# Kernel tuning notes

Measured on AMD Instinct MI355X. Metric: run time of the kernel, lower is better.

## Reference

```python
import jax, jax.numpy as jnp
import numpy as np

N, E, G = 20000, 320000, 256
FXD, FXT, OD = 78, 954, 128


def _lin(key, fan_in, fan_out, scale=0.05):
    return jax.random.normal(key, (fan_in, fan_out), dtype=jnp.float32) * scale


def setup_inputs() -> dict:
    key = jax.random.key(0)
    ks = jax.random.split(key, 24)
    inp = {
        "x1": jax.random.normal(ks[0], (N, FXD), dtype=jnp.float32),
        "edge_index1": jax.random.randint(ks[1], (2, E), 0, N, dtype=jnp.int32),
        "batch1": (jnp.arange(N, dtype=jnp.int32) * G) // N,  # sorted, every graph non-empty
        "x2": jax.random.normal(ks[2], (N, FXD), dtype=jnp.float32),
        "edge_index2": jax.random.randint(ks[3], (2, E), 0, N, dtype=jnp.int32),
        "batch2": (jnp.arange(N, dtype=jnp.int32) * G) // N,
        "cell": jax.random.normal(ks[4], (G, FXT), dtype=jnp.float32),
        # GCNConv weights (shared across the two drug branches, as in the module)
        "Wc1": _lin(ks[5], FXD, FXD), "bc1": jnp.zeros((FXD,), jnp.float32),
        "Wc2": _lin(ks[6], FXD, FXD * 2), "bc2": jnp.zeros((FXD * 2,), jnp.float32),
        "Wc3": _lin(ks[7], FXD * 2, FXD * 4), "bc3": jnp.zeros((FXD * 4,), jnp.float32),
        "Wg1": _lin(ks[8], FXD * 4, FXD * 2), "bg1": jnp.zeros((FXD * 2,), jnp.float32),
        "Wg2": _lin(ks[9], FXD * 2, OD), "bg2": jnp.zeros((OD,), jnp.float32),
        # cell reduction MLP 954 -> 2048 -> 512 -> 256
        "Wr1": _lin(ks[10], FXT, 2048), "br1": jnp.zeros((2048,), jnp.float32),
        "Wr2": _lin(ks[11], 2048, 512), "br2": jnp.zeros((512,), jnp.float32),
        "Wr3": _lin(ks[12], 512, OD * 2), "br3": jnp.zeros((OD * 2,), jnp.float32),
        # head MLP 512 -> 1024 -> 512 -> 128 -> 2
        "Wf1": _lin(ks[13], OD * 4, 1024), "bf1": jnp.zeros((1024,), jnp.float32),
        "Wf2": _lin(ks[14], 1024, 512), "bf2": jnp.zeros((512,), jnp.float32),
        "Wf3": _lin(ks[15], 512, 128), "bf3": jnp.zeros((128,), jnp.float32),
        "Wo": _lin(ks[16], 128, 2), "bo": jnp.zeros((2,), jnp.float32),
    }
    return inp


def gcn_conv(x, W, b, src, dst, n):
    """PyG GCNConv: h = D^{-1/2}(A+I)D^{-1/2} (x W) + b (self-loops added)."""
    h = x @ W
    loops = jnp.arange(n, dtype=src.dtype)
    s = jnp.concatenate([src, loops])
    d = jnp.concatenate([dst, loops])
    deg = jax.ops.segment_sum(jnp.ones_like(s, dtype=h.dtype), d, num_segments=n)
    dinv = jax.lax.rsqrt(deg)  # deg >= 1 due to self-loops
    norm = dinv[s] * dinv[d]  # [E+N]
    out = jax.ops.segment_sum(h[s] * norm[:, None], d, num_segments=n)
    return out + b


def drug_branch(x, ei, batch, Wc1, bc1, Wc2, bc2, Wc3, bc3, Wg1, bg1, Wg2, bg2):
    src, dst = ei[0], ei[1]
    n = x.shape[0]
    x = jax.nn.relu(gcn_conv(x, Wc1, bc1, src, dst, n))
    x = jax.nn.relu(gcn_conv(x, Wc2, bc2, src, dst, n))
    x = jax.nn.relu(gcn_conv(x, Wc3, bc3, src, dst, n))
    x = jax.ops.segment_max(x, batch, num_segments=G)  # global max pool -> [G, 312]
    x = jax.nn.relu(x @ Wg1 + bg1)
    x = x @ Wg2 + bg2  # dropout is identity in eval mode
    return x


def reference(x1, edge_index1, batch1, x2, edge_index2, batch2, cell,
              Wc1, bc1, Wc2, bc2, Wc3, bc3, Wg1, bg1, Wg2, bg2,
              Wr1, br1, Wr2, br2, Wr3, br3,
              Wf1, bf1, Wf2, bf2, Wf3, bf3, Wo, bo):
    g1 = drug_branch(x1, edge_index1, batch1, Wc1, bc1, Wc2, bc2, Wc3, bc3, Wg1, bg1, Wg2, bg2)
    g2 = drug_branch(x2, edge_index2, batch2, Wc1, bc1, Wc2, bc2, Wc3, bc3, Wg1, bg1, Wg2, bg2)
    # F.normalize(cell, p=2, dim=1)
    cv = cell / jnp.maximum(jnp.linalg.norm(cell, axis=1, keepdims=True), 1e-12)
    cv = jax.nn.relu(cv @ Wr1 + br1)
    cv = jax.nn.relu(cv @ Wr2 + br2)
    cv = jax.nn.relu(cv @ Wr3 + br3)
    xc = jnp.concatenate([g1, g2, cv], axis=1)  # [G, 512]
    xc = jax.nn.relu(xc @ Wf1 + bf1)
    xc = jax.nn.relu(xc @ Wf2 + bf2)
    xc = jax.nn.relu(xc @ Wf3 + bf3)
    return xc @ Wo + bo  # [G, 2]
```

## Files before the change

kernel.cpp:

```cpp
#include <hip/hip_runtime.h>

#define N_NODES 20000
#define N_EDGES 320000
#define N_GRAPH 256
#define ECHUNK 2048
#define DCAP 64

__device__ __forceinline__ ushort f2b(float f) {
  unsigned u = __float_as_uint(f);
  u += 0x7FFFu + ((u >> 16) & 1u);
  return (ushort)(u >> 16);
}
__device__ __forceinline__ float b2f(ushort u) {
  return __uint_as_float(((unsigned)u) << 16);
}

typedef __attribute__((ext_vector_type(8))) short bf16x8;
typedef __attribute__((ext_vector_type(4))) float f32x4;

__device__ __forceinline__ void acc8(float* a, uint4 u) {
  a[0] += __uint_as_float(u.x << 16);
  a[1] += __uint_as_float(u.x & 0xFFFF0000u);
  a[2] += __uint_as_float(u.y << 16);
  a[3] += __uint_as_float(u.y & 0xFFFF0000u);
  a[4] += __uint_as_float(u.z << 16);
  a[5] += __uint_as_float(u.z & 0xFFFF0000u);
  a[6] += __uint_as_float(u.w << 16);
  a[7] += __uint_as_float(u.w & 0xFFFF0000u);
}

template <int BN_T>
__launch_bounds__(256)
__global__ void gemm_fused(const ushort* __restrict__ h,
                           const int* __restrict__ cnt,
                           const ushort* __restrict__ col_idx,
                           const float* __restrict__ dinv,
                           const ushort* __restrict__ Bt, int ldbt,
                           ushort* __restrict__ C, int ldc,
                           const float* __restrict__ bias,
                           int Nr, int M, int cwz) {
  constexpr int BM = 64, BN = BN_T * 16, LA = 104;
  __shared__ __align__(16) ushort Afull[BM][LA];
  __shared__ __align__(16) ushort Bsl[BN][40];
  const int tid = threadIdx.x;
  const int R = (Nr + BM - 1) / BM;
  const int RR = (R + 7) >> 3;
  const int xz = blockIdx.x & 7, g = blockIdx.x >> 3;
  const int by = xz * RR + g;
  if (by >= R) return;
  const int row0 = by * BM;
  const int lane = tid & 63, w = tid >> 6;
  const uint4* hv = (const uint4*)h;

  for (int task = tid; task < BM * 10; task += 256) {
    const int r = task / 10, c = task - r * 10;
    const int n = row0 + r;
    uint4 val = make_uint4(0u, 0u, 0u, 0u);
    if (n < Nr) {
      float a[8] = {};
      acc8(a, hv[(size_t)n * 10 + c]);
      const int beg = n << 6;
      const int end = beg + min(cnt[n], DCAP);
      int e = beg;
      for (; e + 3 < end; e += 4) {
        int s0 = col_idx[e], s1 = col_idx[e + 1];
        int s2 = col_idx[e + 2], s3 = col_idx[e + 3];
        acc8(a, hv[(size_t)s0 * 10 + c]); acc8(a, hv[(size_t)s1 * 10 + c]);
        acc8(a, hv[(size_t)s2 * 10 + c]); acc8(a, hv[(size_t)s3 * 10 + c]);
      }
      for (; e < end; ++e) acc8(a, hv[(size_t)col_idx[e] * 10 + c]);
      const float dn = dinv[n];
      ushort o[8];
#pragma unroll
      for (int j = 0; j < 8; ++j) o[j] = f2b(dn * a[j]);
      val = *(uint4*)o;
    }
    *(uint4*)&Afull[r][c * 8] = val;
  }
  for (int task = tid; task < BM * 2; task += 256) {
    const int r = task >> 1, c2 = task & 1;
    *(uint4*)&Afull[r][80 + c2 * 8] = make_uint4(0u, 0u, 0u, 0u);
  }
  __syncthreads();

  f32x4 acc[BN_T] = {};
  const int mrow = w * 16;
  const int lm = lane & 15, lq = (lane >> 4) * 8;
  for (int t = 0; t < 3; ++t) {
    const int k0 = t * 32;
    for (int s = tid; s < BN * 4; s += 256) {
      const int br = s >> 2, bo = (s & 3) * 8;
      *(uint4*)&Bsl[br][bo] = *(const uint4*)&Bt[(size_t)br * ldbt + k0 + bo];
    }
    __syncthreads();
    bf16x8 af = *(const bf16x8*)&Afull[mrow + lm][k0 + lq];
#pragma unroll
    for (int nt = 0; nt < BN_T; ++nt) {
      bf16x8 bf = *(const bf16x8*)&Bsl[nt * 16 + lm][lq];
      acc[nt] = __builtin_amdgcn_mfma_f32_16x16x32_bf16(af, bf, acc[nt], 0, 0, 0);
    }
    __syncthreads();
  }

  const int rquad = (lane >> 4) * 4;
#pragma unroll
  for (int nt = 0; nt < BN_T; ++nt) {
    const int cc = nt * 16 + lm;
    if (cc >= cwz) continue;
    const bool cval = cc < M;
    const float bv = cval ? bias[cc] : 0.f;
#pragma unroll
    for (int r = 0; r < 4; ++r) {
      const int rr = row0 + mrow + rquad + r;
      if (rr >= Nr) continue;
      float v = cval ? fmaxf(acc[nt][r] + bv, 0.f) * dinv[rr] : 0.f;
      C[(size_t)rr * ldc + cc] = f2b(v);
    }
  }
}

template <int POOL>
__launch_bounds__(256)
__global__ void gemm_mfma(const ushort* __restrict__ A, int lda,
                          const ushort* __restrict__ Bt, int ldbt,
                          void* __restrict__ Cv, int ldc,
                          const float* __restrict__ bias,
                          int Nr, int Kpad, int M, int do_relu, int obf,
                          const float* __restrict__ dsc, int cwz,
                          const int* __restrict__ bA, const int* __restrict__ bB,
                          int nsplit, int gA, int gB, int gTot) {
  constexpr int BM = 128, BN = 128, BK = 32, LK = 40;
  __shared__ __align__(16) ushort Asl[BM][LK];
  __shared__ __align__(16) ushort Bsl[BN][LK];
  const int tid = threadIdx.x;
  const int Cc = (M + BN - 1) / BN;
  const int R = (Nr + BM - 1) / BM;
  const int RR = (R + 7) >> 3;
  const int xz = blockIdx.x & 7, g = blockIdx.x >> 3;
  const int q = g / Cc;
  const int by = xz * RR + q, bx = g - q * Cc;
  if (by >= R) return;
  const int row0 = by * BM, col0 = bx * BN;

  const int lane = tid & 63, w = tid >> 6;
  const int a_r = tid >> 1, a_h = tid & 1;

  const int nst = Kpad / BK;

  uint4 pa0, pa1, pb0, pb1;
  auto load_tile = [&](int k0) {
    if (row0 + a_r < Nr) {
      const uint4* p = (const uint4*)(A + (size_t)(row0 + a_r) * lda + k0 + a_h * 16);
      pa0 = p[0]; pa1 = p[1];
    } else {
      pa0 = make_uint4(0u, 0u, 0u, 0u); pa1 = pa0;
    }
    const uint4* pq = (const uint4*)(Bt + (size_t)(col0 + a_r) * ldbt + k0 + a_h * 16);
    pb0 = pq[0]; pb1 = pq[1];
  };
  auto commit = [&]() {
    *(uint4*)&Asl[a_r][a_h * 16] = pa0;
    *(uint4*)&Asl[a_r][a_h * 16 + 8] = pa1;
    *(uint4*)&Bsl[a_r][a_h * 16] = pb0;
    *(uint4*)&Bsl[a_r][a_h * 16 + 8] = pb1;
  };

  f32x4 acc[2][8] = {};
  const int mrow = w * 32;
  const int lm = lane & 15, lq = (lane >> 4) * 8;

  load_tile(0);
  for (int t = 0; t < nst; ++t) {
    commit();
    __syncthreads();
    if (t + 1 < nst) load_tile((t + 1) * BK);
    bf16x8 af0 = *(const bf16x8*)&Asl[mrow + lm][lq];
    bf16x8 af1 = *(const bf16x8*)&Asl[mrow + 16 + lm][lq];
#pragma unroll
    for (int nt = 0; nt < 8; ++nt) {
      bf16x8 bf = *(const bf16x8*)&Bsl[nt * 16 + lm][lq];
      acc[0][nt] = __builtin_amdgcn_mfma_f32_16x16x32_bf16(af0, bf, acc[0][nt], 0, 0, 0);
      acc[1][nt] = __builtin_amdgcn_mfma_f32_16x16x32_bf16(af1, bf, acc[1][nt], 0, 0, 0);
    }
    __syncthreads();
  }

  const int rquad = (lane >> 4) * 4;

  if constexpr (POOL) {
    __shared__ int Ps[4][BN];
    for (int idx = tid; idx < 4 * BN; idx += 256) Ps[idx >> 7][idx & 127] = 0;
    __syncthreads();
    const int g0 = (row0 < nsplit) ? gA + bA[row0] : gB + bB[row0 - nsplit];
    int gr8[2][4];
#pragma unroll
    for (int mt = 0; mt < 2; ++mt)
#pragma unroll
      for (int r = 0; r < 4; ++r) {
        const int rr = row0 + mrow + mt * 16 + rquad + r;
        gr8[mt][r] = (rr < Nr)
                         ? ((rr < nsplit) ? gA + bA[rr] : gB + bB[rr - nsplit])
                         : -1;
      }
#pragma unroll
    for (int mt = 0; mt < 2; ++mt)
#pragma unroll
      for (int nt = 0; nt < 8; ++nt) {
        const int cl = nt * 16 + lm;
        if (col0 + cl >= M) continue;
        const float bv = bias[col0 + cl];
#pragma unroll
        for (int r = 0; r < 4; ++r) {
          const int gg = gr8[mt][r];
          if (gg < 0) continue;
          const float v = fmaxf(acc[mt][nt][r] + bv, 0.f);
          atomicMax(&Ps[gg - g0][cl], __float_as_int(v));
        }
      }
    __syncthreads();
    for (int idx = tid; idx < 4 * BN; idx += 256) {
      const int s = idx >> 7, c = idx & 127;
      const int gg = g0 + s, cc = col0 + c;
      if (gg < gTot && cc < M)
        atomicMax((int*)Cv + (size_t)gg * ldc + cc, Ps[s][c]);
    }
    return;
  }

  const int cz = (cwz > M) ? cwz : M;
#pragma unroll
  for (int mt = 0; mt < 2; ++mt) {
#pragma unroll
    for (int nt = 0; nt < 8; ++nt) {
      const int cc = col0 + nt * 16 + lm;
      if (cc >= cz) continue;
      const bool cval = cc < M;
      const float bv = (cval && bias) ? bias[cc] : 0.f;
#pragma unroll
      for (int r = 0; r < 4; ++r) {
        const int rr = row0 + mrow + mt * 16 + rquad + r;
        if (rr >= Nr) continue;
        float v = cval ? (acc[mt][nt][r] + bv) : 0.f;
        if (do_relu) v = fmaxf(v, 0.f);
        if (dsc) v *= dsc[rr];
        if (obf) ((ushort*)Cv)[(size_t)rr * ldc + cc] = f2b(v);
        else     ((float*)Cv)[(size_t)rr * ldc + cc] = v;
      }
    }
  }
}

struct GJob {
  const void* A; const ushort* Bt; void* C; const float* bias;
  int lda, a_f32, ldbt, ldc, Nr, Kpad, M, relu, obf, rsplit, cpad, rb, cb, blk0;
};

__launch_bounds__(256)
__global__ void gemm_grp(GJob j0, GJob j1, int njobs) {
  GJob j = (njobs > 1 && (int)blockIdx.x >= j1.blk0) ? j1 : j0;
  const int local = blockIdx.x - j.blk0;
  const int by = local / j.cb, bx = local - by * j.cb;
  const int row0 = by * 32, col0 = bx * 64;
  const int tid = threadIdx.x, lane = tid & 63, w = tid >> 6;

  __shared__ __align__(16) char smem[32768];
  ushort (*Asl)[32][40] = (ushort (*)[32][40])smem;
  ushort (*Bsl)[64][40] = (ushort (*)[64][40])(smem + 10240);
  float  (*Rs)[32][64]  = (float  (*)[32][64])smem;

  const int a_r = lane >> 1, a_h = lane & 1;
  const int lm = lane & 15, lq = (lane >> 4) * 8;
  const int nst = j.Kpad / 32;

  uint4 ra[4], rb[4];
  auto gload = [&](int t) {
    const int k0 = t * 32;
    const int ar = row0 + a_r;
    if (j.a_f32) {
      if (ar < j.Nr) {
        const uint4* p = (const uint4*)((const float*)j.A + (size_t)ar * j.lda + k0 + a_h * 16);
        ra[0] = p[0]; ra[1] = p[1]; ra[2] = p[2]; ra[3] = p[3];
      } else {
        ra[0] = make_uint4(0u, 0u, 0u, 0u); ra[1] = ra[0]; ra[2] = ra[0]; ra[3] = ra[0];
      }
    } else {
      if (ar < j.Nr) {
        const uint4* p = (const uint4*)((const ushort*)j.A + (size_t)ar * j.lda + k0 + a_h * 16);
        ra[0] = p[0]; ra[1] = p[1];
      } else {
        ra[0] = make_uint4(0u, 0u, 0u, 0u); ra[1] = ra[0];
      }
    }
    const uint4* q = (const uint4*)(j.Bt + (size_t)(col0 + lane) * j.ldbt + k0);
    rb[0] = q[0]; rb[1] = q[1]; rb[2] = q[2]; rb[3] = q[3];
  };
  auto commit = [&]() {
    if (j.a_f32) {
      ushort tmp[16];
      const float* f = (const float*)&ra[0];
#pragma unroll
      for (int q2 = 0; q2 < 16; ++q2) tmp[q2] = f2b(f[q2]);
      *(uint4*)&Asl[w][a_r][a_h * 16]     = *(uint4*)&tmp[0];
      *(uint4*)&Asl[w][a_r][a_h * 16 + 8] = *(uint4*)&tmp[8];
    } else {
      *(uint4*)&Asl[w][a_r][a_h * 16]     = ra[0];
      *(uint4*)&Asl[w][a_r][a_h * 16 + 8] = ra[1];
    }
    *(uint4*)&Bsl[w][lane][0]  = rb[0];
    *(uint4*)&Bsl[w][lane][8]  = rb[1];
    *(uint4*)&Bsl[w][lane][16] = rb[2];
    *(uint4*)&Bsl[w][lane][24] = rb[3];
  };

  f32x4 acc[2][4] = {};
  if (w < nst) {
    gload(w);
    for (int t = w; t < nst; t += 4) {
      commit();
      bf16x8 af0 = *(const bf16x8*)&Asl[w][lm][lq];
      bf16x8 af1 = *(const bf16x8*)&Asl[w][16 + lm][lq];
      bf16x8 bq0 = *(const bf16x8*)&Bsl[w][lm][lq];
      bf16x8 bq1 = *(const bf16x8*)&Bsl[w][16 + lm][lq];
      bf16x8 bq2 = *(const bf16x8*)&Bsl[w][32 + lm][lq];
      bf16x8 bq3 = *(const bf16x8*)&Bsl[w][48 + lm][lq];
      if (t + 4 < nst) gload(t + 4);
      acc[0][0] = __builtin_amdgcn_mfma_f32_16x16x32_bf16(af0, bq0, acc[0][0], 0, 0, 0);
      acc[0][1] = __builtin_amdgcn_mfma_f32_16x16x32_bf16(af0, bq1, acc[0][1], 0, 0, 0);
      acc[0][2] = __builtin_amdgcn_mfma_f32_16x16x32_bf16(af0, bq2, acc[0][2], 0, 0, 0);
      acc[0][3] = __builtin_amdgcn_mfma_f32_16x16x32_bf16(af0, bq3, acc[0][3], 0, 0, 0);
      acc[1][0] = __builtin_amdgcn_mfma_f32_16x16x32_bf16(af1, bq0, acc[1][0], 0, 0, 0);
      acc[1][1] = __builtin_amdgcn_mfma_f32_16x16x32_bf16(af1, bq1, acc[1][1], 0, 0, 0);
      acc[1][2] = __builtin_amdgcn_mfma_f32_16x16x32_bf16(af1, bq2, acc[1][2], 0, 0, 0);
      acc[1][3] = __builtin_amdgcn_mfma_f32_16x16x32_bf16(af1, bq3, acc[1][3], 0, 0, 0);
    }
  }

  __syncthreads();
  const int rquad = (lane >> 4) * 4;
#pragma unroll
  for (int mt = 0; mt < 2; ++mt)
#pragma unroll
    for (int nt = 0; nt < 4; ++nt)
#pragma unroll
      for (int r = 0; r < 4; ++r)
        Rs[w][mt * 16 + rquad + r][nt * 16 + lm] = acc[mt][nt][r];
  __syncthreads();

  const int rrow = tid >> 3, cs = (tid & 7) * 8;
  float v[8];
  {
    float4 x0 = *(const float4*)&Rs[0][rrow][cs];
    float4 x1 = *(const float4*)&Rs[0][rrow][cs + 4];
    v[0] = x0.x; v[1] = x0.y; v[2] = x0.z; v[3] = x0.w;
    v[4] = x1.x; v[5] = x1.y; v[6] = x1.z; v[7] = x1.w;
  }
#pragma unroll
  for (int ww = 1; ww < 4; ++ww) {
    float4 x0 = *(const float4*)&Rs[ww][rrow][cs];
    float4 x1 = *(const float4*)&Rs[ww][rrow][cs + 4];
    v[0] += x0.x; v[1] += x0.y; v[2] += x0.z; v[3] += x0.w;
    v[4] += x1.x; v[5] += x1.y; v[6] += x1.z; v[7] += x1.w;
  }
  const int rg = row0 + rrow;
  if (rg < j.Nr) {
    int rm = rg, rq = 0;
    if (j.rsplit) { rq = rg / j.rsplit; rm = rg - rq * j.rsplit; }
#pragma unroll
    for (int q = 0; q < 8; ++q) {
      const int cc = col0 + cs + q;
      if (cc >= j.cpad) break;
      float x = 0.f;
      if (cc < j.M) {
        x = v[q] + j.bias[cc];
        if (j.relu) x = fmaxf(x, 0.f);
      }
      const size_t di = (size_t)rm * j.ldc + (size_t)rq * j.M + cc;
      if (j.obf) ((ushort*)j.C)[di] = f2b(x);
      else       ((float*)j.C)[di] = x;
    }
  }
}

struct WJob { const float* W; ushort* T; int Mv, Kv, Mp, Kp, blk0; };
struct WArgs {
  WJob j[11]; int wblocks; const float* cell; ushort* cv;
  const int* e1; const int* e2; int* cnt; ushort* col; int E, npass, rng, scatB;
};

__launch_bounds__(256)
__global__ void prep_all(WArgs a) {
  const int bid = blockIdx.x, tid = threadIdx.x;
  if (bid < a.wblocks) {
    __shared__ float t[32][33];
    int ji = 0;
#pragma unroll
    for (int i = 1; i < 11; ++i)
      if (bid >= a.j[i].blk0) ji = i;
    WJob wj = a.j[ji];
    const int lt = bid - wj.blk0;
    const int ktiles = wj.Kp >> 5;
    const int tn = lt / ktiles, tk = lt - tn * ktiles;
    const int n0 = tn << 5, k0 = tk << 5;
    const int c = tid & 31, r = tid >> 5;
    const int nn = n0 + c;
#pragma unroll
    for (int i = 0; i < 4; ++i) {
      const int k = k0 + r + i * 8;
      t[r + i * 8][c] = (k < wj.Kv && nn < wj.Mv) ? wj.W[(size_t)k * wj.Mv + nn] : 0.f;
    }
    __syncthreads();
    const int k = k0 + c;
#pragma unroll
    for (int i = 0; i < 4; ++i) {
      const int n = n0 + r + i * 8;
      wj.T[(size_t)n * wj.Kp + k] = f2b(t[c][r + i * 8]);
    }
    return;
  }
  if (bid < a.wblocks + N_GRAPH) {
    __shared__ float red[256];
    const int g = bid - a.wblocks;
    const float* row = a.cell + (size_t)g * 954;
    float s = 0.f;
    for (int f = tid; f < 954; f += 256) { float vv = row[f]; s += vv * vv; }
    red[tid] = s;
    __syncthreads();
    for (int off2 = 128; off2 > 0; off2 >>= 1) {
      if (tid < off2) red[tid] += red[tid + off2];
      __syncthreads();
    }
    const float inv = 1.f / fmaxf(sqrtf(red[0]), 1e-12f);
    ushort* orow = a.cv + (size_t)g * 960;
    for (int f = tid; f < 954; f += 256) orow[f] = f2b(row[f] * inv);
    for (int f = 954 + tid; f < 960; f += 256) orow[f] = 0;
    return;
  }
  const int sb = bid - a.wblocks - N_GRAPH;
  const int xcd = sb & 7;
  const int lo = xcd * a.rng, hi = lo + a.rng;
  const int base = (sb >> 3) * ECHUNK;
  const int TE = a.npass * a.E;
  for (int i = tid; i < ECHUNK; i += 256) {
    int e = base + i;
    if (e >= TE) break;
    int d, s;
    if (e < a.E) { d = a.e1[a.E + e]; s = a.e1[e]; }
    else { int jj = e - a.E; d = N_NODES + a.e2[a.E + jj]; s = N_NODES + a.e2[jj]; }
    if (d >= lo && d < hi) {
      int p = atomicAdd(&a.cnt[d], 1);
      if (p < DCAP) a.col[((size_t)d << 6) + p] = (ushort)s;
    }
  }
}

__global__ void scatterb_kernel(const int* __restrict__ e1, const int* __restrict__ e2,
                                int* __restrict__ cnt, ushort* __restrict__ col_idx,
                                int E, int npass, int rng) {
  const int xcd = blockIdx.x & 7;
  const int lo = xcd * rng, hi = lo + rng;
  const int base = (blockIdx.x >> 3) * ECHUNK;
  const int TE = npass * E;
  for (int i = threadIdx.x; i < ECHUNK; i += 256) {
    int e = base + i;
    if (e >= TE) break;
    int d, s;
    if (e < E) { d = e1[E + e]; s = e1[e]; }
    else { int jj = e - E; d = N_NODES + e2[E + jj]; s = N_NODES + e2[jj]; }
    if (d >= lo && d < hi) {
      int p = atomicAdd(&cnt[d], 1);
      if (p < DCAP) col_idx[((size_t)d << 6) + p] = (ushort)s;
    }
  }
}

__global__ void dinv_cvt_kernel(const int* __restrict__ cnt, float* __restrict__ dinv,
                                const float* __restrict__ xa, const float* __restrict__ xb,
                                int nsplit, ushort* __restrict__ dst, int total) {
  int gid = blockIdx.x * blockDim.x + threadIdx.x;
  if (gid >= total) return;
  int n = gid / 10, v = gid - n * 10;
  const float sc = rsqrtf((float)(cnt[n] + 1));
  if (v == 0) dinv[n] = sc;
  const float* src = (n < nsplit) ? xa + (size_t)n * 78 : xb + (size_t)(n - nsplit) * 78;
  const int f0 = v * 8;
  ushort o[8];
#pragma unroll
  for (int jj = 0; jj < 8; ++jj)
    o[jj] = (f0 + jj < 78) ? f2b(src[f0 + jj] * sc) : 0;
  ((uint4*)(dst + (size_t)n * 80))[v] = *(uint4*)o;
}

__global__ void aggb_flat(const ushort* __restrict__ h, const int* __restrict__ cnt,
                          const ushort* __restrict__ col_idx, const float* __restrict__ dinv,
                          ushort* __restrict__ out, int in_ld, int out_ld,
                          int V, int total) {
  int gid = blockIdx.x * blockDim.x + threadIdx.x;
  if (gid >= total) return;
  int n = gid / V, v = gid - n * V;
  const uint4* hv = (const uint4*)h;
  const int ivs = in_ld >> 3;
  float a[8] = {};
  acc8(a, hv[(size_t)n * ivs + v]);
  const int beg = n << 6;
  const int end = beg + min(cnt[n], DCAP);
  int e = beg;
  for (; e + 3 < end; e += 4) {
    int s0 = col_idx[e], s1 = col_idx[e + 1], s2 = col_idx[e + 2], s3 = col_idx[e + 3];
    uint4 u0 = hv[(size_t)s0 * ivs + v], u1 = hv[(size_t)s1 * ivs + v];
    uint4 u2 = hv[(size_t)s2 * ivs + v], u3 = hv[(size_t)s3 * ivs + v];
    acc8(a, u0); acc8(a, u1); acc8(a, u2); acc8(a, u3);
  }
  for (; e < end; ++e)
    acc8(a, hv[(size_t)col_idx[e] * ivs + v]);
  const float din = dinv[n];
  ushort o[8];
#pragma unroll
  for (int jj = 0; jj < 8; ++jj) o[jj] = f2b(din * a[jj]);
  ((uint4*)(out + (size_t)n * out_ld))[v] = *(uint4*)o;
}

__global__ void wo_kernel(const float* __restrict__ wf3o, const float* __restrict__ Wo,
                          const float* __restrict__ bo, float* __restrict__ out) {
  int gid = blockIdx.x * blockDim.x + threadIdx.x;
  if (gid >= N_GRAPH * 2) return;
  int row = gid >> 1, col = gid & 1;
  float v = bo[col];
  const float* a = wf3o + (size_t)row * 128;
  for (int k = 0; k < 128; ++k) v += a[k] * Wo[k * 2 + col];
  out[gid] = v;
}

extern "C" void kernel_launch(void* const* d_in, const int* in_sizes, int n_in,
                              void* d_out, int out_size, void* d_ws, size_t ws_size,
                              hipStream_t stream) {
  (void)in_sizes; (void)n_in; (void)out_size;
  const float* x1  = (const float*)d_in[0];
  const int*   ei1 = (const int*)d_in[1];
  const int*   bt1 = (const int*)d_in[2];
  const float* x2  = (const float*)d_in[3];
  const int*   ei2 = (const int*)d_in[4];
  const int*   bt2 = (const int*)d_in[5];
  const float* cell = (const float*)d_in[6];
  const float* Wc1 = (const float*)d_in[7];  const float* bc1 = (const float*)d_in[8];
  const float* Wc2 = (const float*)d_in[9];  const float* bc2 = (const float*)d_in[10];
  const float* Wc3 = (const float*)d_in[11]; const float* bc3 = (const float*)d_in[12];
  const float* Wg1 = (const float*)d_in[13]; const float* bg1 = (const float*)d_in[14];
  const float* Wg2 = (const float*)d_in[15]; const float* bg2 = (const float*)d_in[16];
  const float* Wr1 = (const float*)d_in[17]; const float* br1 = (const float*)d_in[18];
  const float* Wr2 = (const float*)d_in[19]; const float* br2 = (const float*)d_in[20];
  const float* Wr3 = (const float*)d_in[21]; const float* br3 = (const float*)d_in[22];
  const float* Wf1 = (const float*)d_in[23]; const float* bf1 = (const float*)d_in[24];
  const float* Wf2 = (const float*)d_in[25]; const float* bf2 = (const float*)d_in[26];
  const float* Wf3 = (const float*)d_in[27]; const float* bf3 = (const float*)d_in[28];
  const float* Wo  = (const float*)d_in[29]; const float* bo  = (const float*)d_in[30];
  float* out = (float*)d_out;

  const bool batched = ws_size >= (size_t)95 * 1024 * 1024;
  const int NPASS = batched ? 2 : 1;
  const int NN = NPASS * N_NODES;

  char* ws = (char*)d_ws;
  size_t off = 0;
  auto alloc_f = [&](size_t ne) {
    ne = (ne + 3) & ~(size_t)3;
    float* p = (float*)(ws + off); off += ne * 4; return p;
  };
  auto alloc_i = [&](size_t ne) {
    ne = (ne + 3) & ~(size_t)3;
    int* p = (int*)(ws + off); off += ne * 4; return p;
  };
  ushort* xb16w = (ushort*)alloc_f((size_t)NN * 80);
  ushort* ab16  = (ushort*)alloc_f((size_t)NN * 80);
  ushort* xb16s = (ushort*)alloc_f((size_t)NN * 40);
  float* dinv   = alloc_f(NN);
  int* cnt      = alloc_i(NN);
  float* pooled = alloc_f((size_t)512 * 320);
  ushort* cv16  = (ushort*)alloc_f((size_t)N_GRAPH * 480);
  ushort* wg1o  = (ushort*)alloc_f((size_t)512 * 80);
  ushort* wr1o  = (ushort*)alloc_f((size_t)256 * 1024);
  ushort* wr2o  = (ushort*)alloc_f((size_t)256 * 256);
  ushort* catbuf = (ushort*)alloc_f((size_t)256 * 256);
  ushort* wf1o  = (ushort*)alloc_f((size_t)256 * 512);
  ushort* wf2o  = (ushort*)alloc_f((size_t)256 * 256);
  float* wf3o   = alloc_f((size_t)256 * 128);
  ushort* wc1t  = (ushort*)alloc_f(128 * 96 / 2);
  ushort* wc2t  = (ushort*)alloc_f(192 * 96 / 2);
  ushort* wc3t  = (ushort*)alloc_f(384 * 160 / 2);
  ushort* wr1t  = (ushort*)alloc_f(2048 * 960 / 2);
  ushort* wr2t  = (ushort*)alloc_f(512 * 2048 / 2);
  ushort* wf1t  = (ushort*)alloc_f(1024 * 512 / 2);
  ushort* wg1t  = (ushort*)alloc_f(192 * 320 / 2);
  ushort* wg2t  = (ushort*)alloc_f(128 * 160 / 2);
  ushort* wr3t  = (ushort*)alloc_f(256 * 512 / 2);
  ushort* wf2t  = (ushort*)alloc_f(512 * 1024 / 2);
  ushort* wf3t  = (ushort*)alloc_f(128 * 512 / 2);
  ushort* col_idx = (ushort*)alloc_i((size_t)NN * DCAP / 2);

  auto mfma_pool = [&](const ushort* A, int lda, const ushort* Bt, int ldbt,
                       const float* bias, int Nr, int Kpad, int M,
                       const int* bA, const int* bB, int nsplit, int gA, int gB, int gTot) {
    int Cc = (M + 127) / 128, R = (Nr + 127) / 128, RR = (R + 7) >> 3;
    dim3 grid(8 * RR * Cc, 1, 1);
    gemm_mfma<1><<<grid, 256, 0, stream>>>(A, lda, Bt, ldbt, pooled, 320, bias,
                                           Nr, Kpad, M, 1, 0, nullptr, 0,
                                           bA, bB, nsplit, gA, gB, gTot);
  };
  auto mkjob = [&](const void* A, int lda, int a_f32, const ushort* Bt, int ldbt,
                   void* C, int ldc, const float* bias, int Nr, int Kpad, int M,
                   int relu, int obf, int rsplit, int cpad) {
    GJob g; g.A = A; g.Bt = Bt; g.C = C; g.bias = bias;
    g.lda = lda; g.a_f32 = a_f32; g.ldbt = ldbt; g.ldc = ldc;
    g.Nr = Nr; g.Kpad = Kpad; g.M = M; g.relu = relu; g.obf = obf;
    g.rsplit = rsplit; g.cpad = cpad;
    g.rb = (Nr + 31) / 32; g.cb = (M + 63) / 64; g.blk0 = 0;
    return g;
  };
  auto grp1 = [&](GJob a) {
    gemm_grp<<<a.rb * a.cb, 256, 0, stream>>>(a, a, 1);
  };
  auto grp2 = [&](GJob a, GJob b) {
    b.blk0 = a.rb * a.cb;
    gemm_grp<<<b.blk0 + b.rb * b.cb, 256, 0, stream>>>(a, b, 2);
  };

  WArgs wa{};
  int wb = 0;
  {
    int nj = 0;
    auto addw = [&](const float* W, ushort* T, int Mv, int Kv, int Mp, int Kp) {
      wa.j[nj].W = W; wa.j[nj].T = T; wa.j[nj].Mv = Mv; wa.j[nj].Kv = Kv;
      wa.j[nj].Mp = Mp; wa.j[nj].Kp = Kp; wa.j[nj].blk0 = wb;
      wb += (Mp >> 5) * (Kp >> 5); ++nj;
    };
    addw(Wc1, wc1t,   78,   78,  128,   96);
    addw(Wc2, wc2t,  156,   78,  192,   96);
    addw(Wc3, wc3t,  312,  156,  384,  160);
    addw(Wr1, wr1t, 2048,  954, 2048,  960);
    addw(Wr2, wr2t,  512, 2048,  512, 2048);
    addw(Wf1, wf1t, 1024,  512, 1024,  512);
    addw(Wg1, wg1t,  156,  312,  192,  320);
    addw(Wg2, wg2t,  128,  156,  128,  160);
    addw(Wr3, wr3t,  256,  512,  256,  512);
    addw(Wf2, wf2t,  512, 1024,  512, 1024);
    addw(Wf3, wf3t,  128,  512,  128,  512);
    wa.wblocks = wb; wa.cell = cell; wa.cv = cv16;
  }

  auto node_layers = [&](const float* xa, const float* xb,
                         const int* bta, const int* btb, int npass, int pool_base) {
    const int nn = npass * N_NODES;
    {
      int tot = nn * 10;
      dinv_cvt_kernel<<<(tot + 255) / 256, 256, 0, stream>>>(
          cnt, dinv, xa, xb, (npass == 2) ? N_NODES : nn, xb16s, tot);
    }
    const int R = (nn + 63) / 64, RR = (R + 7) >> 3;
    dim3 fgrid(8 * RR, 1, 1);
    gemm_fused<8><<<fgrid, 256, 0, stream>>>(xb16s, cnt, col_idx, dinv, wc1t, 96,
                                             (ushort*)ab16, 80, bc1, nn, 78, 80);
    gemm_fused<12><<<fgrid, 256, 0, stream>>>((ushort*)ab16, cnt, col_idx, dinv, wc2t, 96,
                                              xb16w, 160, bc2, nn, 156, 160);
    {
      int tot = nn * 20;
      aggb_flat<<<(tot + 255) / 256, 256, 0, stream>>>(xb16w, cnt, col_idx, dinv,
                                                       (ushort*)ab16, 160, 160, 20, tot);
    }
    mfma_pool((ushort*)ab16, 160, wc3t, 160, bc3, nn, 160, 312,
              bta, btb, (npass == 2) ? N_NODES : nn,
              pool_base, pool_base + N_GRAPH, pool_base + npass * N_GRAPH);
  };

  if (batched) {
    const int echunks = (2 * N_EDGES + ECHUNK - 1) / ECHUNK;
    hipMemsetAsync(cnt, 0, (size_t)NN * 4 + (size_t)512 * 320 * 4, stream);
    wa.e1 = ei1; wa.e2 = ei2; wa.cnt = cnt; wa.col = col_idx;
    wa.E = N_EDGES; wa.npass = 2; wa.rng = NN / 8; wa.scatB = 8 * echunks;
    prep_all<<<wb + N_GRAPH + wa.scatB, 256, 0, stream>>>(wa);
    node_layers(x1, x2, bt1, bt2, 2, 0);
  } else {
    wa.e1 = ei1; wa.e2 = ei1; wa.cnt = cnt; wa.col = col_idx;
    wa.E = N_EDGES; wa.npass = 1; wa.rng = N_NODES / 8; wa.scatB = 0;
    prep_all<<<wb + N_GRAPH, 256, 0, stream>>>(wa);
    const int echunks = (N_EDGES + ECHUNK - 1) / ECHUNK;
    hipMemsetAsync(cnt, 0, (size_t)N_NODES * 4 + (size_t)512 * 320 * 4, stream);
    scatterb_kernel<<<8 * echunks, 256, 0, stream>>>(ei1, ei1, cnt, col_idx,
                                                     N_EDGES, 1, N_NODES / 8);
    node_layers(x1, x1, bt1, bt1, 1, 0);
    hipMemsetAsync(cnt, 0, (size_t)N_NODES * 4, stream);
    scatterb_kernel<<<8 * echunks, 256, 0, stream>>>(ei2, ei2, cnt, col_idx,
                                                     N_EDGES, 1, N_NODES / 8);
    node_layers(x2, x2, bt2, bt2, 1, N_GRAPH);
  }

  grp2(mkjob(pooled, 320, 1, wg1t, 320, wg1o, 160, bg1, 512, 320, 156, 1, 1, 0, 160),
       mkjob(cv16,   960, 0, wr1t, 960, wr1o, 2048, br1, 256, 960, 2048, 1, 1, 0, 2048));
  grp2(mkjob(wg1o,  160, 0, wg2t,  160, catbuf, 512, bg2, 512,  160,  128, 0, 1, 256, 128),
       mkjob(wr1o, 2048, 0, wr2t, 2048, wr2o,   512, br2, 256, 2048,  512, 1, 1, 0, 512));
  grp1(mkjob(wr2o, 512, 0, wr3t, 512, catbuf + 256, 512, br3, 256, 512, 256, 1, 1, 0, 256));
  grp1(mkjob(catbuf, 512, 0, wf1t,  512, wf1o, 1024, bf1, 256,  512, 1024, 1, 1, 0, 1024));
  grp1(mkjob(wf1o,  1024, 0, wf2t, 1024, wf2o,  512, bf2, 256, 1024,  512, 1, 1, 0, 512));
  grp1(mkjob(wf2o,   512, 0, wf3t,  512, wf3o,  128, bf3, 256,  512,  128, 1, 0, 0, 128));
  wo_kernel<<<2, 256, 0, stream>>>(wf3o, Wo, bo, out);
}
```

Measured before the change: 368.6 us.

## Fuse layer-3 aggregation into pooled GEMM and merge MLP tail into cooperative kernel

Replaces the separate aggregation kernel and the 128x128 pooled MFMA GEMM with one kernel. Each block aggregates neighbours for 64 rows into shared memory, then multiplies them against all 320 output columns and max-pools into graphs. The six grouped MLP launches plus the output kernel become one cooperative kernel that uses grid.sync between levels, which removes launch overhead. The costs are larger shared memory use and higher register pressure (20 accumulators), the weight matrix being re-streamed by every block, and a cooperative launch with 256 blocks that may lower tail parallelism.

Result: slower. 625.9 us (+69.8%).

```diff
diff --git a/kernel.cpp b/kernel.cpp
--- a/kernel.cpp
+++ b/kernel.cpp
@@ -1,4 +1,7 @@
 #include <hip/hip_runtime.h>
+#include <hip/hip_cooperative_groups.h>
+
+namespace cg = cooperative_groups;
 
 #define N_NODES 20000
 #define N_EDGES 320000
@@ -119,134 +122,105 @@
   }
 }
 
-template <int POOL>
 __launch_bounds__(256)
-__global__ void gemm_mfma(const ushort* __restrict__ A, int lda,
-                          const ushort* __restrict__ Bt, int ldbt,
-                          void* __restrict__ Cv, int ldc,
-                          const float* __restrict__ bias,
-                          int Nr, int Kpad, int M, int do_relu, int obf,
-                          const float* __restrict__ dsc, int cwz,
-                          const int* __restrict__ bA, const int* __restrict__ bB,
-                          int nsplit, int gA, int gB, int gTot) {
-  constexpr int BM = 128, BN = 128, BK = 32, LK = 40;
-  __shared__ __align__(16) ushort Asl[BM][LK];
-  __shared__ __align__(16) ushort Bsl[BN][LK];
+__global__ void gemm_fused3(const ushort* __restrict__ h,
+                            const int* __restrict__ cnt,
+                            const ushort* __restrict__ col_idx,
+                            const float* __restrict__ dinv,
+                            const ushort* __restrict__ Bt, int ldbt,
+                            int* __restrict__ pooled, int ldp,
+                            const float* __restrict__ bias,
+                            int Nr, int M,
+                            const int* __restrict__ bA, const int* __restrict__ bB,
+                            int nsplit, int gA, int gB, int gTot) {
+  constexpr int BM = 64, BN = 320, LA = 168;
+  __shared__ __align__(16) ushort Afull[BM][LA];
+  __shared__ __align__(16) ushort Bsl[BN][40];
+  __shared__ int Ps[2][BN];
   const int tid = threadIdx.x;
-  const int Cc = (M + BN - 1) / BN;
   const int R = (Nr + BM - 1) / BM;
   const int RR = (R + 7) >> 3;
   const int xz = blockIdx.x & 7, g = blockIdx.x >> 3;
-  const int q = g / Cc;
-  const int by = xz * RR + q, bx = g - q * Cc;
+  const int by = xz * RR + g;
   if (by >= R) return;
-  const int row0 = by * BM, col0 = bx * BN;
-
+  const int row0 = by * BM;
   const int lane = tid & 63, w = tid >> 6;
-  const int a_r = tid >> 1, a_h = tid & 1;
-
-  const int nst = Kpad / BK;
-
-  uint4 pa0, pa1, pb0, pb1;
-  auto load_tile = [&](int k0) {
-    if (row0 + a_r < Nr) {
-      const uint4* p = (const uint4*)(A + (size_t)(row0 + a_r) * lda + k0 + a_h * 16);
-      pa0 = p[0]; pa1 = p[1];
-    } else {
-      pa0 = make_uint4(0u, 0u, 0u, 0u); pa1 = pa0;
-    }
-    const uint4* pq = (const uint4*)(Bt + (size_t)(col0 + a_r) * ldbt + k0 + a_h * 16);
-    pb0 = pq[0]; pb1 = pq[1];
-  };
-  auto commit = [&]() {
-    *(uint4*)&Asl[a_r][a_h * 16] = pa0;
-    *(uint4*)&Asl[a_r][a_h * 16 + 8] = pa1;
-    *(uint4*)&Bsl[a_r][a_h * 16] = pb0;
-    *(uint4*)&Bsl[a_r][a_h * 16 + 8] = pb1;
-  };
-
-  f32x4 acc[2][8] = {};
-  const int mrow = w * 32;
+  const uint4* hv = (const uint4*)h;
+
+  for (int task = tid; task < BM * 20; task += 256) {
+    const int r = task / 20, c = task - r * 20;
+    const int n = row0 + r;
+    uint4 val = make_uint4(0u, 0u, 0u, 0u);
+    if (n < Nr) {
+      float a[8] = {};
+      acc8(a, hv[(size_t)n * 20 + c]);
+      const int beg = n << 6;
+      const int end = beg + min(cnt[n], DCAP);
+      int e = beg;
+      for (; e + 3 < end; e += 4) {
+        int s0 = col_idx[e], s1 = col_idx[e + 1];
+        int s2 = col_idx[e + 2], s3 = col_idx[e + 3];
+        acc8(a, hv[(size_t)s0 * 20 + c]); acc8(a, hv[(size_t)s1 * 20 + c]);
+        acc8(a, hv[(size_t)s2 * 20 + c]); acc8(a, hv[(size_t)s3 * 20 + c]);
+      }
+      for (; e < end; ++e) acc8(a, hv[(size_t)col_idx[e] * 20 + c]);
+      const float dn = dinv[n];
+      ushort o[8];
+#pragma unroll
+      for (int j = 0; j < 8; ++j) o[j] = f2b(dn * a[j]);
+      val = *(uint4*)o;
+    }
+    *(uint4*)&Afull[r][c * 8] = val;
+  }
+  for (int idx = tid; idx < 2 * BN; idx += 256) ((int*)Ps)[idx] = 0;
+  __syncthreads();
+
+  f32x4 acc[20] = {};
+  const int mrow = w * 16;
   const int lm = lane & 15, lq = (lane >> 4) * 8;
-
-  load_tile(0);
-  for (int t = 0; t < nst; ++t) {
-    commit();
+  for (int t = 0; t < 5; ++t) {
+    const int k0 = t * 32;
+    for (int s = tid; s < BN * 4; s += 256) {
+      const int br = s >> 2, bo = (s & 3) * 8;
+      *(uint4*)&Bsl[br][bo] = *(const uint4*)&Bt[(size_t)br * ldbt + k0 + bo];
+    }
     __syncthreads();
-    if (t + 1 < nst) load_tile((t + 1) * BK);
-    bf16x8 af0 = *(const bf16x8*)&Asl[mrow + lm][lq];
-    bf16x8 af1 = *(const bf16x8*)&Asl[mrow + 16 + lm][lq];
-#pragma unroll
-    for (int nt = 0; nt < 8; ++nt) {
+    bf16x8 af = *(const bf16x8*)&Afull[mrow + lm][k0 + lq];
+#pragma unroll
+    for (int nt = 0; nt < 20; ++nt) {
       bf16x8 bf = *(const bf16x8*)&Bsl[nt * 16 + lm][lq];
-      acc[0][nt] = __builtin_amdgcn_mfma_f32_16x16x32_bf16(af0, bf, acc[0][nt], 0, 0, 0);
-      acc[1][nt] = __builtin_amdgcn_mfma_f32_16x16x32_bf16(af1, bf, acc[1][nt], 0, 0, 0);
+      acc[nt] = __builtin_amdgcn_mfma_f32_16x16x32_bf16(af, bf, acc[nt], 0, 0, 0);
     }
     __syncthreads();
   }
 
   const int rquad = (lane >> 4) * 4;
-
-  if constexpr (POOL) {
-    __shared__ int Ps[4][BN];
-    for (int idx = tid; idx < 4 * BN; idx += 256) Ps[idx >> 7][idx & 127] = 0;
-    __syncthreads();
-    const int g0 = (row0 < nsplit) ? gA + bA[row0] : gB + bB[row0 - nsplit];
-    int gr8[2][4];
-#pragma unroll
-    for (int mt = 0; mt < 2; ++mt)
-#pragma unroll
-      for (int r = 0; r < 4; ++r) {
-        const int rr = row0 + mrow + mt * 16 + rquad + r;
-        gr8[mt][r] = (rr < Nr)
-                         ? ((rr < nsplit) ? gA + bA[rr] : gB + bB[rr - nsplit])
-                         : -1;
-      }
-#pragma unroll
-    for (int mt = 0; mt < 2; ++mt)
-#pragma unroll
-      for (int nt = 0; nt < 8; ++nt) {
-        const int cl = nt * 16 + lm;
-        if (col0 + cl >= M) continue;
-        const float bv = bias[col0 + cl];
-#pragma unroll
-        for (int r = 0; r < 4; ++r) {
-          const int gg = gr8[mt][r];
-          if (gg < 0) continue;
-          const float v = fmaxf(acc[mt][nt][r] + bv, 0.f);
-          atomicMax(&Ps[gg - g0][cl], __float_as_int(v));
-        }
-      }
-    __syncthreads();
-    for (int idx = tid; idx < 4 * BN; idx += 256) {
-      const int s = idx >> 7, c = idx & 127;
-      const int gg = g0 + s, cc = col0 + c;
-      if (gg < gTot && cc < M)
-        atomicMax((int*)Cv + (size_t)gg * ldc + cc, Ps[s][c]);
-    }
-    return;
-  }
-
-  const int cz = (cwz > M) ? cwz : M;
-#pragma unroll
-  for (int mt = 0; mt < 2; ++mt) {
-#pragma unroll
-    for (int nt = 0; nt < 8; ++nt) {
-      const int cc = col0 + nt * 16 + lm;
-      if (cc >= cz) continue;
-      const bool cval = cc < M;
-      const float bv = (cval && bias) ? bias[cc] : 0.f;
-#pragma unroll
-      for (int r = 0; r < 4; ++r) {
-        const int rr = row0 + mrow + mt * 16 + rquad + r;
-        if (rr >= Nr) continue;
-        float v = cval ? (acc[mt][nt][r] + bv) : 0.f;
-        if (do_relu) v = fmaxf(v, 0.f);
-        if (dsc) v *= dsc[rr];
-        if (obf) ((ushort*)Cv)[(size_t)rr * ldc + cc] = f2b(v);
-        else     ((float*)Cv)[(size_t)rr * ldc + cc] = v;
-      }
-    }
+  const int g0 = (row0 < nsplit) ? gA + bA[row0] : gB + bB[row0 - nsplit];
+  int gr[4];
+#pragma unroll
+  for (int r = 0; r < 4; ++r) {
+    const int rr = row0 + mrow + rquad + r;
+    gr[r] = (rr < Nr) ? ((rr < nsplit) ? gA + bA[rr] : gB + bB[rr - nsplit]) - g0 : -1;
+  }
+#pragma unroll
+  for (int nt = 0; nt < 20; ++nt) {
+    const int cc = nt * 16 + lm;
+    if (cc >= M) continue;
+    const float bv = bias[cc];
+#pragma unroll
+    for (int r = 0; r < 4; ++r) {
+      if (gr[r] < 0) continue;
+      const float v = fmaxf(acc[nt][r] + bv, 0.f);
+      atomicMax(&Ps[gr[r]][cc], __float_as_int(v));
+    }
+  }
+  __syncthreads();
+  for (int idx = tid; idx < 2 * BN; idx += 256) {
+    const int s = (idx >= BN) ? 1 : 0;
+    const int c = idx - s * BN;
+    const int gg = g0 + s;
+    if (gg < gTot && c < M)
+      atomicMax(pooled + (size_t)gg * ldp + c, Ps[s][c]);
   }
 }
 
@@ -255,15 +229,11 @@
   int lda, a_f32, ldbt, ldc, Nr, Kpad, M, relu, obf, rsplit, cpad, rb, cb, blk0;
 };
 
-__launch_bounds__(256)
-__global__ void gemm_grp(GJob j0, GJob j1, int njobs) {
-  GJob j = (njobs > 1 && (int)blockIdx.x >= j1.blk0) ? j1 : j0;
-  const int local = blockIdx.x - j.blk0;
+__device__ void tail_tile(const GJob& j, int local, char* smem) {
   const int by = local / j.cb, bx = local - by * j.cb;
   const int row0 = by * 32, col0 = bx * 64;
   const int tid = threadIdx.x, lane = tid & 63, w = tid >> 6;
 
-  __shared__ __align__(16) char smem[32768];
   ushort (*Asl)[32][40] = (ushort (*)[32][40])smem;
   ushort (*Bsl)[64][40] = (ushort (*)[64][40])(smem + 10240);
   float  (*Rs)[32][64]  = (float  (*)[32][64])smem;
@@ -379,6 +349,38 @@
       else       ((float*)j.C)[di] = x;
     }
   }
+  __syncthreads();
+}
+
+struct TailArgs {
+  GJob j[8];
+  const float* wf3o; const float* Wo; const float* bo; float* out;
+};
+
+__launch_bounds__(256)
+__global__ void mlp_tail(TailArgs ta) {
+  __shared__ __align__(16) char smem[32768];
+  cg::grid_group grid = cg::this_grid();
+  const int lv_lo[6] = {0, 2, 4, 5, 6, 7};
+  const int lv_hi[6] = {2, 4, 5, 6, 7, 8};
+  for (int lv = 0; lv < 6; ++lv) {
+    int tot = 0;
+    for (int ji = lv_lo[lv]; ji < lv_hi[lv]; ++ji) tot += ta.j[ji].rb * ta.j[ji].cb;
+    for (int t = blockIdx.x; t < tot; t += gridDim.x) {
+      int ji = lv_lo[lv], rem = t;
+      while (rem >= ta.j[ji].rb * ta.j[ji].cb) { rem -= ta.j[ji].rb * ta.j[ji].cb; ++ji; }
+      tail_tile(ta.j[ji], rem, smem);
+    }
+    grid.sync();
+  }
+  const int gid = blockIdx.x * 256 + threadIdx.x;
+  if (gid < N_GRAPH * 2) {
+    const int row = gid >> 1, col = gid & 1;
+    float v = ta.bo[col];
+    const float* a = ta.wf3o + (size_t)row * 128;
+    for (int k = 0; k < 128; ++k) v += a[k] * ta.Wo[k * 2 + col];
+    ta.out[gid] = v;
+  }
 }
 
 struct WJob { const float* W; ushort* T; int Mv, Kv, Mp, Kp, blk0; };
@@ -488,46 +490,6 @@
   for (int jj = 0; jj < 8; ++jj)
     o[jj] = (f0 + jj < 78) ? f2b(src[f0 + jj] * sc) : 0;
   ((uint4*)(dst + (size_t)n * 80))[v] = *(uint4*)o;
-}
-
-__global__ void aggb_flat(const ushort* __restrict__ h, const int* __restrict__ cnt,
-                          const ushort* __restrict__ col_idx, const float* __restrict__ dinv,
-                          ushort* __restrict__ out, int in_ld, int out_ld,
-                          int V, int total) {
-  int gid = blockIdx.x * blockDim.x + threadIdx.x;
-  if (gid >= total) return;
-  int n = gid / V, v = gid - n * V;
-  const uint4* hv = (const uint4*)h;
-  const int ivs = in_ld >> 3;
-  float a[8] = {};
-  acc8(a, hv[(size_t)n * ivs + v]);
-  const int beg = n << 6;
-  const int end = beg + min(cnt[n], DCAP);
-  int e = beg;
-  for (; e + 3 < end; e += 4) {
-    int s0 = col_idx[e], s1 = col_idx[e + 1], s2 = col_idx[e + 2], s3 = col_idx[e + 3];
-    uint4 u0 = hv[(size_t)s0 * ivs + v], u1 = hv[(size_t)s1 * ivs + v];
-    uint4 u2 = hv[(size_t)s2 * ivs + v], u3 = hv[(size_t)s3 * ivs + v];
-    acc8(a, u0); acc8(a, u1); acc8(a, u2); acc8(a, u3);
-  }
-  for (; e < end; ++e)
-    acc8(a, hv[(size_t)col_idx[e] * ivs + v]);
-  const float din = dinv[n];
-  ushort o[8];
-#pragma unroll
-  for (int jj = 0; jj < 8; ++jj) o[jj] = f2b(din * a[jj]);
-  ((uint4*)(out + (size_t)n * out_ld))[v] = *(uint4*)o;
-}
-
-__global__ void wo_kernel(const float* __restrict__ wf3o, const float* __restrict__ Wo,
-                          const float* __restrict__ bo, float* __restrict__ out) {
-  int gid = blockIdx.x * blockDim.x + threadIdx.x;
-  if (gid >= N_GRAPH * 2) return;
-  int row = gid >> 1, col = gid & 1;
-  float v = bo[col];
-  const float* a = wf3o + (size_t)row * 128;
-  for (int k = 0; k < 128; ++k) v += a[k] * Wo[k * 2 + col];
-  out[gid] = v;
 }
 
 extern "C" void kernel_launch(void* const* d_in, const int* in_sizes, int n_in,
@@ -556,8 +518,9 @@
   float* out = (float*)d_out;
 
   const bool batched = ws_size >= (size_t)95 * 1024 * 1024;
+  const int NN = batched ? 2 * N_NODES : N_NODES;
   const int NPASS = batched ? 2 : 1;
-  const int NN = NPASS * N_NODES;
+  const int NNW = NPASS * N_NODES;
 
   char* ws = (char*)d_ws;
   size_t off = 0;
@@ -569,11 +532,11 @@
     ne = (ne + 3) & ~(size_t)3;
     int* p = (int*)(ws + off); off += ne * 4; return p;
   };
-  ushort* xb16w = (ushort*)alloc_f((size_t)NN * 80);
-  ushort* ab16  = (ushort*)alloc_f((size_t)NN * 80);
-  ushort* xb16s = (ushort*)alloc_f((size_t)NN * 40);
-  float* dinv   = alloc_f(NN);
-  int* cnt      = alloc_i(NN);
+  ushort* xb16w = (ushort*)alloc_f((size_t)NNW * 80);
+  ushort* ab16  = (ushort*)alloc_f((size_t)NNW * 40);
+  ushort* xb16s = (ushort*)alloc_f((size_t)NNW * 40);
+  float* dinv   = alloc_f(NNW);
+  int* cnt      = alloc_i(NNW);
   float* pooled = alloc_f((size_t)512 * 320);
   ushort* cv16  = (ushort*)alloc_f((size_t)N_GRAPH * 480);
   ushort* wg1o  = (ushort*)alloc_f((size_t)512 * 80);
@@ -595,16 +558,8 @@
   ushort* wf2t  = (ushort*)alloc_f(512 * 1024 / 2);
   ushort* wf3t  = (ushort*)alloc_f(128 * 512 / 2);
   ushort* col_idx = (ushort*)alloc_i((size_t)NN * DCAP / 2);
-
-  auto mfma_pool = [&](const ushort* A, int lda, const ushort* Bt, int ldbt,
-                       const float* bias, int Nr, int Kpad, int M,
-                       const int* bA, const int* bB, int nsplit, int gA, int gB, int gTot) {
-    int Cc = (M + 127) / 128, R = (Nr + 127) / 128, RR = (R + 7) >> 3;
-    dim3 grid(8 * RR * Cc, 1, 1);
-    gemm_mfma<1><<<grid, 256, 0, stream>>>(A, lda, Bt, ldbt, pooled, 320, bias,
-                                           Nr, Kpad, M, 1, 0, nullptr, 0,
-                                           bA, bB, nsplit, gA, gB, gTot);
-  };
+  (void)NN;
+
   auto mkjob = [&](const void* A, int lda, int a_f32, const ushort* Bt, int ldbt,
                    void* C, int ldc, const float* bias, int Nr, int Kpad, int M,
                    int relu, int obf, int rsplit, int cpad) {
@@ -614,13 +569,6 @@
     g.rsplit = rsplit; g.cpad = cpad;
     g.rb = (Nr + 31) / 32; g.cb = (M + 63) / 64; g.blk0 = 0;
     return g;
-  };
-  auto grp1 = [&](GJob a) {
-    gemm_grp<<<a.rb * a.cb, 256, 0, stream>>>(a, a, 1);
-  };
-  auto grp2 = [&](GJob a, GJob b) {
-    b.blk0 = a.rb * a.cb;
-    gemm_grp<<<b.blk0 + b.rb * b.cb, 256, 0, stream>>>(a, b, 2);
   };
 
   WArgs wa{};
@@ -657,24 +605,21 @@
     const int R = (nn + 63) / 64, RR = (R + 7) >> 3;
     dim3 fgrid(8 * RR, 1, 1);
     gemm_fused<8><<<fgrid, 256, 0, stream>>>(xb16s, cnt, col_idx, dinv, wc1t, 96,
-                                             (ushort*)ab16, 80, bc1, nn, 78, 80);
-    gemm_fused<12><<<fgrid, 256, 0, stream>>>((ushort*)ab16, cnt, col_idx, dinv, wc2t, 96,
+                                             ab16, 80, bc1, nn, 78, 80);
+    gemm_fused<12><<<fgrid, 256, 0, stream>>>(ab16, cnt, col_idx, dinv, wc2t, 96,
                                               xb16w, 160, bc2, nn, 156, 160);
-    {
-      int tot = nn * 20;
-      aggb_flat<<<(tot + 255) / 256, 256, 0, stream>>>(xb16w, cnt, col_idx, dinv,
-                                                       (ushort*)ab16, 160, 160, 20, tot);
-    }
-    mfma_pool((ushort*)ab16, 160, wc3t, 160, bc3, nn, 160, 312,
-              bta, btb, (npass == 2) ? N_NODES : nn,
-              pool_base, pool_base + N_GRAPH, pool_base + npass * N_GRAPH);
+    gemm_fused3<<<fgrid, 256, 0, stream>>>(xb16w, cnt, col_idx, dinv, wc3t, 160,
+                                           (int*)pooled, 320, bc3, nn, 312,
+                                           bta, btb, (npass == 2) ? N_NODES : nn,
+                                           pool_base, pool_base + N_GRAPH,
+                                           pool_base + npass * N_GRAPH);
   };
 
   if (batched) {
     const int echunks = (2 * N_EDGES + ECHUNK - 1) / ECHUNK;
-    hipMemsetAsync(cnt, 0, (size_t)NN * 4 + (size_t)512 * 320 * 4, stream);
+    hipMemsetAsync(cnt, 0, (size_t)NNW * 4 + (size_t)512 * 320 * 4, stream);
     wa.e1 = ei1; wa.e2 = ei2; wa.cnt = cnt; wa.col = col_idx;
-    wa.E = N_EDGES; wa.npass = 2; wa.rng = NN / 8; wa.scatB = 8 * echunks;
+    wa.E = N_EDGES; wa.npass = 2; wa.rng = NNW / 8; wa.scatB = 8 * echunks;
     prep_all<<<wb + N_GRAPH + wa.scatB, 256, 0, stream>>>(wa);
     node_layers(x1, x2, bt1, bt2, 2, 0);
   } else {
@@ -692,13 +637,18 @@
     node_layers(x2, x2, bt2, bt2, 1, N_GRAPH);
   }
 
-  grp2(mkjob(pooled, 320, 1, wg1t, 320, wg1o, 160, bg1, 512, 320, 156, 1, 1, 0, 160),
-       mkjob(cv16,   960, 0, wr1t, 960, wr1o, 2048, br1, 256, 960, 2048, 1, 1, 0, 2048));
-  grp2(mkjob(wg1o,  160, 0, wg2t,  160, catbuf, 512, bg2, 512,  160,  128, 0, 1, 256, 128),
-       mkjob(wr1o, 2048, 0, wr2t, 2048, wr2o,   512, br2, 256, 2048,  512, 1, 1, 0, 512));
-  grp1(mkjob(wr2o, 512, 0, wr3t, 512, catbuf + 256, 512, br3, 256, 512, 256, 1, 1, 0, 256));
-  grp1(mkjob(catbuf, 512, 0, wf1t,  512, wf1o, 1024, bf1, 256,  512, 1024, 1, 1, 0, 1024));
-  grp1(mkjob(wf1o,  1024, 0, wf2t, 1024, wf2o,  512, bf2, 256, 1024,  512, 1, 1, 0, 512));
-  grp1(mkjob(wf2o,   512, 0, wf3t,  512, wf3o,  128, bf3, 256,  512,  128, 1, 0, 0, 128));
-  wo_kernel<<<2, 256, 0, stream>>>(wf3o, Wo, bo, out);
-}
+  {
+    TailArgs ta{};
+    ta.j[0] = mkjob(pooled, 320, 1, wg1t, 320, wg1o, 160, bg1, 512, 320, 156, 1, 1, 0, 160);
+    ta.j[1] = mkjob(cv16,   960, 0, wr1t, 960, wr1o, 2048, br1, 256, 960, 2048, 1, 1, 0, 2048);
+    ta.j[2] = mkjob(wg1o,  160, 0, wg2t,  160, catbuf, 512, bg2, 512,  160,  128, 0, 1, 256, 128);
+    ta.j[3] = mkjob(wr1o, 2048, 0, wr2t, 2048, wr2o,   512, br2, 256, 2048,  512, 1, 1, 0, 512);
+    ta.j[4] = mkjob(wr2o,  512, 0, wr3t,  512, catbuf + 256, 512, br3, 256, 512, 256, 1, 1, 0, 256);
+    ta.j[5] = mkjob(catbuf, 512, 0, wf1t,  512, wf1o, 1024, bf1, 256,  512, 1024, 1, 1, 0, 1024);
+    ta.j[6] = mkjob(wf1o,  1024, 0, wf2t, 1024, wf2o,  512, bf2, 256, 1024,  512, 1, 1, 0, 512);
+    ta.j[7] = mkjob(wf2o,   512, 0, wf3t,  512, wf3o,  128, bf3, 256,  512,  128, 1, 0, 0, 128);
+    ta.wf3o = wf3o; ta.Wo = Wo; ta.bo = bo; ta.out = out;
+    void* kargs[] = { &ta };
+    hipLaunchCooperativeKernel((void*)mlp_tail, dim3(256), dim3(256), kargs, 0, stream);
+  }
+}
```
